# Performance work log

Measured on AMD Instinct MI355X. Metric: run time of the kernel, lower is better.

The kernel has to match this reference:

```python
import jax, jax.numpy as jnp
import numpy as np

NUM_EMBEDDINGS = 1024
EMBEDDING_DIM = 64
COMMITMENT_COST = 0.25


def setup_inputs() -> dict:
    key = jax.random.key(0)
    k1, k2 = jax.random.split(key)
    inputs = jax.random.normal(k1, (64, 32, 32, EMBEDDING_DIM), dtype=jnp.float32)
    # torch init is uniform(-1/K, 1/K); scale accordingly
    weight = jax.random.uniform(
        k2, (NUM_EMBEDDINGS, EMBEDDING_DIM), dtype=jnp.float32,
        minval=-1.0 / NUM_EMBEDDINGS, maxval=1.0 / NUM_EMBEDDINGS)
    return {"inputs": inputs, "weight": weight}


def reference(inputs, weight):
    input_shape = inputs.shape
    flat = inputs.reshape(-1, EMBEDDING_DIM)               # [N, D]
    distances = (jnp.sum(flat ** 2, axis=1, keepdims=True)
                 + jnp.sum(weight ** 2, axis=1)
                 - 2.0 * flat @ weight.T)                   # [N, K]
    encoding_indices = jnp.argmin(distances, axis=1)        # [N]
    # gather codes (equivalent to one-hot @ weight, but as a direct gather)
    quantized = weight[encoding_indices].reshape(input_shape)

    e_latent_loss = jnp.mean((jax.lax.stop_gradient(quantized) - inputs) ** 2)
    q_latent_loss = jnp.mean((quantized - jax.lax.stop_gradient(inputs)) ** 2)
    loss = q_latent_loss + COMMITMENT_COST * e_latent_loss

    # straight-through estimator
    quantized_ste = inputs + jax.lax.stop_gradient(quantized - inputs)

    # perplexity (equivalent to mean over the one-hot encodings)
    n_tokens = flat.shape[0]
    counts = jax.ops.segment_sum(
        jnp.ones((n_tokens,), jnp.float32), encoding_indices,
        num_segments=NUM_EMBEDDINGS)
    avg_probs = counts / n_tokens
    perplexity = jnp.exp(-jnp.sum(avg_probs * jnp.log(avg_probs + 1e-10)))

    indices_for_transformer = encoding_indices.reshape(input_shape[0], -1)
    return (loss, quantized_ste, perplexity, indices_for_transformer)
```

## Files before the change

### kernel.cpp

```cpp
#include <hip/hip_runtime.h>
#include <cstdint>
#include <cstddef>

#define N_TOKENS 65536
#define DIM 64
#define K_CODES 1024
#define NTH 256
#define TPB 128
#define NCH 16

#define OFF_Q 1
#define OFF_PERP 4194305
#define OFF_IDX 4194306

#define MARGIN 1.5e-4f

#define WS_LOSS   0
#define WS_FCNT   8
#define WS_COUNTS 16
#define WS_WHI    4112
#define WS_WLO    135184
#define WS_S2     266256
#define WS_FLIST  270352

typedef __attribute__((ext_vector_type(8))) short  s16x8;
typedef __attribute__((ext_vector_type(4))) float  f32x4;

__device__ __forceinline__ float fmulr(float a, float b){ return __fmul_rn(a,b); }
__device__ __forceinline__ float faddr(float a, float b){ return __fadd_rn(a,b); }

__device__ __forceinline__ unsigned short f2bf(float f) {
    unsigned u = __float_as_uint(f);
    unsigned r = u + 0x7fffu + ((u >> 16) & 1u);
    return (unsigned short)(r >> 16);
}
__device__ __forceinline__ float bf2f(unsigned short h) {
    return __uint_as_float(((unsigned)h) << 16);
}

__device__ float sumsq64_np(const float* __restrict__ p) {
    float s[16];
    #pragma unroll
    for (int l = 0; l < 16; ++l) {
        float a0 = fmulr(p[l],      p[l]);
        float a1 = fmulr(p[l + 16], p[l + 16]);
        float a2 = fmulr(p[l + 32], p[l + 32]);
        float a3 = fmulr(p[l + 48], p[l + 48]);
        s[l] = faddr(faddr(a0, a1), faddr(a2, a3));
    }
    #pragma unroll
    for (int len = 8; len >= 1; len >>= 1)
        #pragma unroll
        for (int l = 0; l < len; ++l)
            s[l] = faddr(s[l], s[l + len]);
    return s[0];
}

__device__ __forceinline__ void async_copy16(const void* g, void* l) {
    __builtin_amdgcn_global_load_lds(
        (const __attribute__((address_space(1))) void*)g,
        (__attribute__((address_space(3))) void*)l, 16, 0, 0);
}

__global__ void vq_prep(const float* __restrict__ W, unsigned short* __restrict__ Whi,
                        unsigned short* __restrict__ Wlo, float* __restrict__ s2g,
                        int* __restrict__ counts, int* __restrict__ gfcount,
                        double* __restrict__ loss_acc) {
    int gid = blockIdx.x * NTH + threadIdx.x;
    for (int e = gid; e < K_CODES * DIM; e += 16384) {
        float x = W[e];
        unsigned short hi = f2bf(x);
        unsigned short lo = f2bf(__fsub_rn(x, bf2f(hi)));
        int j = e >> 6, k = e & 63;
        int pos = j * 64 + (((k >> 3) ^ (j & 7)) << 3) + (k & 7);
        Whi[pos] = hi; Wlo[pos] = lo;
    }
    if (gid < K_CODES) { s2g[gid] = sumsq64_np(W + gid * 64); counts[gid] = 0; }
    if (gid == 0) { *loss_acc = 0.0; *gfcount = 0; }
}

__global__ __launch_bounds__(NTH, 2)
void vq_main(const float* __restrict__ X, const float* __restrict__ W,
             const unsigned short* __restrict__ WhiG, const unsigned short* __restrict__ WloG,
             const float* __restrict__ s2g, float* __restrict__ out,
             double* __restrict__ loss_acc, int* __restrict__ counts,
             int* __restrict__ gfcount, unsigned short* __restrict__ gflist) {
    __shared__ __align__(16) unsigned short xs_hi[TPB * 64];
    __shared__ __align__(16) unsigned short xs_lo[TPB * 64];
    __shared__ __align__(16) unsigned short ws_hi[2][64 * 64];
    __shared__ __align__(16) unsigned short ws_lo[2][64 * 64];
    __shared__ __align__(16) float s2s[K_CODES];
    __shared__ int fidx[TPB];
    __shared__ int flist[TPB];
    __shared__ int fcount, gbaseS;
    __shared__ double lred[4];

    const int tid  = threadIdx.x;
    const int lane = tid & 63, wave = tid >> 6;
    const int quad = lane >> 4, lrow = lane & 15;
    const int t0   = blockIdx.x * TPB;

    if (tid == 0) fcount = 0;

    {
        const char* gh = (const char*)WhiG;
        const char* gl = (const char*)WloG;
        char* lh = (char*)&ws_hi[0][0] + wave * 1024;
        char* ll = (char*)&ws_lo[0][0] + wave * 1024;
        #pragma unroll
        for (int i = 0; i < 2; ++i) {
            async_copy16(gh + i * 4096 + tid * 16, lh + i * 4096);
            async_copy16(gl + i * 4096 + tid * 16, ll + i * 4096);
        }
    }
    *(f32x4*)&s2s[tid * 4] = *(const f32x4*)&s2g[tid * 4];
    #pragma unroll
    for (int i = 0; i < 4; ++i) {
        int g = tid + NTH * i;
        int t = g >> 3, kb = g & 7;
        const float* src = X + (size_t)(t0 + t) * DIM + kb * 8;
        float v[8];
        *(f32x4*)v       = *(const f32x4*)src;
        *(f32x4*)(v + 4) = *(const f32x4*)(src + 4);
        unsigned short h[8], l[8];
        #pragma unroll
        for (int k = 0; k < 8; ++k) {
            h[k] = f2bf(v[k]);
            l[k] = f2bf(__fsub_rn(v[k], bf2f(h[k])));
        }
        int base = t * 64 + ((kb ^ (t & 7)) << 3);
        *(s16x8*)&xs_hi[base] = *(s16x8*)h;
        *(s16x8*)&xs_lo[base] = *(s16x8*)l;
    }
    __syncthreads();

    s16x8 a_h0[2], a_h1[2], a_l0[2], a_l1[2];
    #pragma unroll
    for (int rt = 0; rt < 2; ++rt) {
        int tf = wave * 32 + rt * 16 + lrow;
        int sA = tf & 7;
        a_h0[rt] = *(const s16x8*)&xs_hi[tf * 64 + (((0 + quad) ^ sA) << 3)];
        a_h1[rt] = *(const s16x8*)&xs_hi[tf * 64 + (((4 + quad) ^ sA) << 3)];
        a_l0[rt] = *(const s16x8*)&xs_lo[tf * 64 + (((0 + quad) ^ sA) << 3)];
        a_l1[rt] = *(const s16x8*)&xs_lo[tf * 64 + (((4 + quad) ^ sA) << 3)];
    }

    float r1v[8], r2v[8]; int r1i[8];
    #pragma unroll
    for (int ri = 0; ri < 8; ++ri) { r1v[ri] = 3.4e38f; r2v[ri] = 3.4e38f; r1i[ri] = 0x7fffffff; }

    for (int ch = 0; ch < NCH; ++ch) {
        const int buf = ch & 1;
        if (ch < NCH - 1) {
            const char* gh = (const char*)WhiG + (ch + 1) * 8192;
            const char* gl = (const char*)WloG + (ch + 1) * 8192;
            char* lh = (char*)&ws_hi[buf ^ 1][0] + wave * 1024;
            char* ll = (char*)&ws_lo[buf ^ 1][0] + wave * 1024;
            #pragma unroll
            for (int i = 0; i < 2; ++i) {
                async_copy16(gh + i * 4096 + tid * 16, lh + i * 4096);
                async_copy16(gl + i * 4096 + tid * 16, ll + i * 4096);
            }
        }
        #pragma unroll
        for (int ct = 0; ct < 4; ++ct) {
            int lc = ct * 16 + lrow;
            int sB = lrow & 7;
            const unsigned short* bh = &ws_hi[buf][lc * 64];
            const unsigned short* bl = &ws_lo[buf][lc * 64];
            s16x8 b_h0 = *(const s16x8*)&bh[((0 + quad) ^ sB) << 3];
            s16x8 b_h1 = *(const s16x8*)&bh[((4 + quad) ^ sB) << 3];
            s16x8 b_l0 = *(const s16x8*)&bl[((0 + quad) ^ sB) << 3];
            s16x8 b_l1 = *(const s16x8*)&bl[((4 + quad) ^ sB) << 3];
            int jcode = ch * 64 + lc;
            float s2v = s2s[jcode];
            float ainit = fmulr(-0.5f, s2v);
            #pragma unroll
            for (int rt = 0; rt < 2; ++rt) {
                f32x4 acc = {ainit, ainit, ainit, ainit};
                acc = __builtin_amdgcn_mfma_f32_16x16x32_bf16(a_h0[rt], b_h0, acc, 0, 0, 0);
                acc = __builtin_amdgcn_mfma_f32_16x16x32_bf16(a_h1[rt], b_h1, acc, 0, 0, 0);
                acc = __builtin_amdgcn_mfma_f32_16x16x32_bf16(a_h0[rt], b_l0, acc, 0, 0, 0);
                acc = __builtin_amdgcn_mfma_f32_16x16x32_bf16(a_h1[rt], b_l1, acc, 0, 0, 0);
                acc = __builtin_amdgcn_mfma_f32_16x16x32_bf16(a_l0[rt], b_h0, acc, 0, 0, 0);
                acc = __builtin_amdgcn_mfma_f32_16x16x32_bf16(a_l1[rt], b_h1, acc, 0, 0, 0);
                #pragma unroll
                for (int r = 0; r < 4; ++r) {
                    float d = fmulr(-2.0f, acc[r]);
                    int ri = rt * 4 + r;
                    bool lt = d < r1v[ri];
                    float sec = lt ? r1v[ri] : d;
                    r2v[ri] = fminf(r2v[ri], sec);
                    r1v[ri] = lt ? d : r1v[ri];
                    r1i[ri] = lt ? jcode : r1i[ri];
                }
            }
        }
        __syncthreads();
    }

    #pragma unroll
    for (int m = 1; m <= 8; m <<= 1) {
        #pragma unroll
        for (int ri = 0; ri < 8; ++ri) {
            float o1v = __shfl_xor(r1v[ri], m, 64);
            int   o1i = __shfl_xor(r1i[ri], m, 64);
            float o2v = __shfl_xor(r2v[ri], m, 64);
            bool take = (o1v < r1v[ri]) || (o1v == r1v[ri] && o1i < r1i[ri]);
            float loser = take ? r1v[ri] : o1v;
            r2v[ri] = fminf(fminf(r2v[ri], o2v), loser);
            if (take) { r1v[ri] = o1v; r1i[ri] = o1i; }
        }
    }
    if (lrow == 0) {
        #pragma unroll
        for (int ri = 0; ri < 8; ++ri) {
            int rt = ri >> 2, r = ri & 3;
            int t = wave * 32 + rt * 16 + quad * 4 + r;
            bool fb = (r2v[ri] - r1v[ri]) < MARGIN;
            fidx[t] = fb ? (r1i[ri] | (int)0x80000000) : r1i[ri];
            if (fb) { int p = atomicAdd(&fcount, 1); flist[p] = t; }
        }
    }
    __syncthreads();

    double lsum = 0.0;
    #pragma unroll
    for (int i = 0; i < 8; ++i) {
        int e4 = tid + NTH * i;
        int t = e4 >> 4, d4 = (e4 & 15) * 4;
        int iv = fidx[t];
        if (iv >= 0) {
            f32x4 q = *(const f32x4*)&W[iv * 64 + d4];
            f32x4 x = *(const f32x4*)&X[(size_t)(t0 + t) * 64 + d4];
            *(f32x4*)&out[(size_t)OFF_Q + (size_t)(t0 + t) * 64 + d4] = q;
            #pragma unroll
            for (int c = 0; c < 4; ++c) {
                float df = __fsub_rn(q[c], x[c]);
                lsum += (double)fmulr(df, df);
            }
        }
    }
    #pragma unroll
    for (int off = 32; off >= 1; off >>= 1) lsum += __shfl_down(lsum, off, 64);
    if (lane == 0) lred[wave] = lsum;
    if (tid < TPB) {
        int iv = fidx[tid];
        if (iv >= 0) {
            atomicAdd(&counts[iv], 1);
            out[(size_t)OFF_IDX + t0 + tid] = (float)iv;
        }
    }
    if (tid == 0) gbaseS = atomicAdd(gfcount, fcount);
    __syncthreads();
    if (tid < fcount) gflist[gbaseS + tid] = (unsigned short)(t0 + flist[tid]);
    if (tid == 0) atomicAdd(loss_acc, lred[0] + lred[1] + lred[2] + lred[3]);
}

__global__ __launch_bounds__(NTH, 3)
void vq_fallback(const float* __restrict__ X, const float* __restrict__ W,
                 const float* __restrict__ s2g, const int* __restrict__ gfcount,
                 const unsigned short* __restrict__ gflist, float* __restrict__ out,
                 double* __restrict__ loss_acc, int* __restrict__ counts) {
    int count = *gfcount;
    int base = blockIdx.x * 64;
    if (base >= count) return;
    int nt = min(64, count - base);

    __shared__ __align__(16) float xsf[64 * 64];
    __shared__ __align__(16) float wsf[128 * 64];
    __shared__ float s1f[64];
    __shared__ int gidx[64];
    __shared__ double lredf[4];

    const int tid = threadIdx.x;
    const int lane = tid & 63, wave = tid >> 6;
    const int r = tid & 15, c = tid >> 4;

    #pragma unroll
    for (int i = 0; i < 4; ++i) {
        int idx = tid + NTH * i;
        int t = idx >> 4, kb = idx & 15;
        int tok = gflist[base + (t < nt ? t : 0)];
        f32x4 v = *(const f32x4*)(X + (size_t)tok * 64 + kb * 4);
        *(f32x4*)&xsf[t * 64 + ((kb ^ ((t >> 2) & 7)) << 2)] = v;
    }
    if (tid < nt) s1f[tid] = sumsq64_np(X + (size_t)gflist[base + tid] * 64);

    float runVal[4]; int runIdx[4];
    #pragma unroll
    for (int i = 0; i < 4; ++i) { runVal[i] = 3.4e38f; runIdx[i] = 0; }

    for (int ch = 0; ch < 8; ++ch) {
        __syncthreads();
        #pragma unroll
        for (int i = 0; i < 8; ++i) {
            int idx = tid + NTH * i;
            int jl = idx >> 4, kb = idx & 15;
            f32x4 v = *(const f32x4*)(W + (size_t)(ch * 128 + jl) * 64 + kb * 4);
            *(f32x4*)&wsf[jl * 64 + ((kb ^ ((jl >> 3) & 7)) << 2)] = v;
        }
        __syncthreads();

        float acc[4][8];
        #pragma unroll
        for (int i = 0; i < 4; ++i)
            #pragma unroll
            for (int m = 0; m < 8; ++m) acc[i][m] = 0.0f;

        #pragma unroll
        for (int kb = 0; kb < 16; ++kb) {
            f32x4 xv[4], wv[8];
            #pragma unroll
            for (int i = 0; i < 4; ++i)
                xv[i] = *(const f32x4*)&xsf[(4 * r + i) * 64 + ((kb ^ (r & 7)) << 2)];
            #pragma unroll
            for (int m = 0; m < 8; ++m)
                wv[m] = *(const f32x4*)&wsf[(8 * c + m) * 64 + ((kb ^ (c & 7)) << 2)];
            #pragma unroll
            for (int i = 0; i < 4; ++i)
                #pragma unroll
                for (int m = 0; m < 8; ++m) {
                    acc[i][m] = __builtin_fmaf(xv[i][0], wv[m][0], acc[i][m]);
                    acc[i][m] = __builtin_fmaf(xv[i][1], wv[m][1], acc[i][m]);
                    acc[i][m] = __builtin_fmaf(xv[i][2], wv[m][2], acc[i][m]);
                    acc[i][m] = __builtin_fmaf(xv[i][3], wv[m][3], acc[i][m]);
                }
        }
        #pragma unroll
        for (int i = 0; i < 4; ++i) {
            float s1v = s1f[4 * r + i];
            #pragma unroll
            for (int m = 0; m < 8; ++m) {
                int jl = 8 * c + m;
                float d = faddr(faddr(s1v, s2g[ch * 128 + jl]), fmulr(-2.0f, acc[i][m]));
                if (d < runVal[i]) { runVal[i] = d; runIdx[i] = ch * 128 + jl; }
            }
        }
    }

    __syncthreads();
    unsigned long long* red = (unsigned long long*)wsf;
    #pragma unroll
    for (int i = 0; i < 4; ++i) {
        unsigned long long pk =
            ((unsigned long long)__float_as_uint(runVal[i]) << 32) |
            (unsigned long long)(unsigned int)runIdx[i];
        red[(4 * r + i) * 16 + c] = pk;
    }
    __syncthreads();
    if (tid < 64) {
        unsigned long long best = red[tid * 16];
        #pragma unroll
        for (int cc = 1; cc < 16; ++cc) {
            unsigned long long v = red[tid * 16 + cc];
            best = (v < best) ? v : best;
        }
        int idx = (int)(best & 0xffffffffu);
        gidx[tid] = idx;
        if (tid < nt) {
            int tok = gflist[base + tid];
            out[(size_t)OFF_IDX + tok] = (float)idx;
            atomicAdd(&counts[idx], 1);
        }
    }
    __syncthreads();
    double lsum = 0.0;
    #pragma unroll
    for (int i = 0; i < 4; ++i) {
        int e4 = tid + NTH * i;
        int t = e4 >> 4, d4 = (e4 & 15) * 4;
        if (t < nt) {
            int tok = gflist[base + t];
            int idx = gidx[t];
            f32x4 q = *(const f32x4*)&W[idx * 64 + d4];
            f32x4 x = *(const f32x4*)&X[(size_t)tok * 64 + d4];
            *(f32x4*)&out[(size_t)OFF_Q + (size_t)tok * 64 + d4] = q;
            #pragma unroll
            for (int cc = 0; cc < 4; ++cc) {
                float df = __fsub_rn(q[cc], x[cc]);
                lsum += (double)fmulr(df, df);
            }
        }
    }
    #pragma unroll
    for (int off = 32; off >= 1; off >>= 1) lsum += __shfl_down(lsum, off, 64);
    if (lane == 0) lredf[wave] = lsum;
    __syncthreads();
    if (tid == 0) atomicAdd(loss_acc, lredf[0] + lredf[1] + lredf[2] + lredf[3]);
}

__global__ void vq_final(const int* __restrict__ counts,
                         const double* __restrict__ loss_acc,
                         float* __restrict__ out) {
    __shared__ double hred[4];
    int tid = threadIdx.x;
    double h = 0.0;
    for (int j = tid; j < K_CODES; j += 256) {
        double p = (double)counts[j] / 65536.0;
        h += p * log(p + 1e-10);
    }
    #pragma unroll
    for (int off = 32; off >= 1; off >>= 1) h += __shfl_down(h, off, 64);
    if ((tid & 63) == 0) hred[tid >> 6] = h;
    __syncthreads();
    if (tid == 0) {
        double H = hred[0] + hred[1] + hred[2] + hred[3];
        out[OFF_PERP] = (float)exp(-H);
        double ls = *loss_acc;
        float Lf = (float)(ls / 4194304.0);
        out[0] = faddr(Lf, fmulr(0.25f, Lf));
    }
}

extern "C" void kernel_launch(void* const* d_in, const int* in_sizes, int n_in,
                              void* d_out, int out_size, void* d_ws, size_t ws_size,
                              hipStream_t stream) {
    const float* X = (const float*)d_in[0];
    const float* W = (const float*)d_in[1];
    float* out = (float*)d_out;
    char* ws = (char*)d_ws;
    double* loss_acc = (double*)(ws + WS_LOSS);
    int* gfcount = (int*)(ws + WS_FCNT);
    int* counts = (int*)(ws + WS_COUNTS);
    unsigned short* Whi = (unsigned short*)(ws + WS_WHI);
    unsigned short* Wlo = (unsigned short*)(ws + WS_WLO);
    float* s2g = (float*)(ws + WS_S2);
    unsigned short* gflist = (unsigned short*)(ws + WS_FLIST);

    vq_prep<<<64, NTH, 0, stream>>>(W, Whi, Wlo, s2g, counts, gfcount, loss_acc);
    vq_main<<<N_TOKENS / TPB, NTH, 0, stream>>>(X, W, Whi, Wlo, s2g, out,
                                                loss_acc, counts, gfcount, gflist);
    vq_fallback<<<N_TOKENS / 64, NTH, 0, stream>>>(X, W, s2g, gfcount, gflist,
                                                   out, loss_acc, counts);
    vq_final<<<1, NTH, 0, stream>>>(counts, loss_acc, out);
}
```

Baseline: 173.2 us.

## Split codebook across two wave groups per block and track max dot

The main kernel grows from 256 to 512 threads. Each group of four waves scans half of every 64-code chunk for the same 128 tokens, and the two halves are merged in shared memory. The per-code multiply by -2 is dropped by tracking the maximum of the offset dot product, with the margin halved to match. This doubles the waves available to hide MFMA and LDS latency at the cost of an extra shared-memory merge, a barrier, and more register pressure under the stricter launch bound.

```diff
diff --git a/kernel.cpp b/kernel.cpp
--- a/kernel.cpp
+++ b/kernel.cpp
@@ -6,6 +6,7 @@
 #define DIM 64
 #define K_CODES 1024
 #define NTH 256
+#define NTHM 512
 #define TPB 128
 #define NCH 16
 
@@ -14,6 +15,7 @@
 #define OFF_IDX 4194306
 
 #define MARGIN 1.5e-4f
+#define HMARGIN 7.5e-5f
 
 #define WS_LOSS   0
 #define WS_FCNT   8
@@ -79,7 +81,7 @@
     if (gid == 0) { *loss_acc = 0.0; *gfcount = 0; }
 }
 
-__global__ __launch_bounds__(NTH, 2)
+__global__ __launch_bounds__(NTHM, 4)
 void vq_main(const float* __restrict__ X, const float* __restrict__ W,
              const unsigned short* __restrict__ WhiG, const unsigned short* __restrict__ WloG,
              const float* __restrict__ s2g, float* __restrict__ out,
@@ -90,14 +92,19 @@
     __shared__ __align__(16) unsigned short ws_hi[2][64 * 64];
     __shared__ __align__(16) unsigned short ws_lo[2][64 * 64];
     __shared__ __align__(16) float s2s[K_CODES];
+    __shared__ float sm1[2][TPB];
+    __shared__ float sm2[2][TPB];
+    __shared__ int   si1[2][TPB];
     __shared__ int fidx[TPB];
     __shared__ int flist[TPB];
     __shared__ int fcount, gbaseS;
-    __shared__ double lred[4];
+    __shared__ double lred[8];
 
     const int tid  = threadIdx.x;
     const int lane = tid & 63, wave = tid >> 6;
     const int quad = lane >> 4, lrow = lane & 15;
+    const int tg   = wave & 3;
+    const int chd  = wave >> 2;
     const int t0   = blockIdx.x * TPB;
 
     if (tid == 0) fcount = 0;
@@ -107,16 +114,13 @@
         const char* gl = (const char*)WloG;
         char* lh = (char*)&ws_hi[0][0] + wave * 1024;
         char* ll = (char*)&ws_lo[0][0] + wave * 1024;
-        #pragma unroll
-        for (int i = 0; i < 2; ++i) {
-            async_copy16(gh + i * 4096 + tid * 16, lh + i * 4096);
-            async_copy16(gl + i * 4096 + tid * 16, ll + i * 4096);
-        }
-    }
-    *(f32x4*)&s2s[tid * 4] = *(const f32x4*)&s2g[tid * 4];
-    #pragma unroll
-    for (int i = 0; i < 4; ++i) {
-        int g = tid + NTH * i;
+        async_copy16(gh + tid * 16, lh);
+        async_copy16(gl + tid * 16, ll);
+    }
+    if (tid < 256) *(f32x4*)&s2s[tid * 4] = *(const f32x4*)&s2g[tid * 4];
+    #pragma unroll
+    for (int i = 0; i < 2; ++i) {
+        int g = tid + NTHM * i;
         int t = g >> 3, kb = g & 7;
         const float* src = X + (size_t)(t0 + t) * DIM + kb * 8;
         float v[8];
@@ -137,7 +141,7 @@
     s16x8 a_h0[2], a_h1[2], a_l0[2], a_l1[2];
     #pragma unroll
     for (int rt = 0; rt < 2; ++rt) {
-        int tf = wave * 32 + rt * 16 + lrow;
+        int tf = tg * 32 + rt * 16 + lrow;
         int sA = tf & 7;
         a_h0[rt] = *(const s16x8*)&xs_hi[tf * 64 + (((0 + quad) ^ sA) << 3)];
         a_h1[rt] = *(const s16x8*)&xs_hi[tf * 64 + (((4 + quad) ^ sA) << 3)];
@@ -145,9 +149,9 @@
         a_l1[rt] = *(const s16x8*)&xs_lo[tf * 64 + (((4 + quad) ^ sA) << 3)];
     }
 
-    float r1v[8], r2v[8]; int r1i[8];
-    #pragma unroll
-    for (int ri = 0; ri < 8; ++ri) { r1v[ri] = 3.4e38f; r2v[ri] = 3.4e38f; r1i[ri] = 0x7fffffff; }
+    float m1v[8], m2v[8]; int m1i[8];
+    #pragma unroll
+    for (int ri = 0; ri < 8; ++ri) { m1v[ri] = -3.4e38f; m2v[ri] = -3.4e38f; m1i[ri] = 0x7fffffff; }
 
     for (int ch = 0; ch < NCH; ++ch) {
         const int buf = ch & 1;
@@ -156,15 +160,12 @@
             const char* gl = (const char*)WloG + (ch + 1) * 8192;
             char* lh = (char*)&ws_hi[buf ^ 1][0] + wave * 1024;
             char* ll = (char*)&ws_lo[buf ^ 1][0] + wave * 1024;
-            #pragma unroll
-            for (int i = 0; i < 2; ++i) {
-                async_copy16(gh + i * 4096 + tid * 16, lh + i * 4096);
-                async_copy16(gl + i * 4096 + tid * 16, ll + i * 4096);
-            }
-        }
-        #pragma unroll
-        for (int ct = 0; ct < 4; ++ct) {
-            int lc = ct * 16 + lrow;
+            async_copy16(gh + tid * 16, lh);
+            async_copy16(gl + tid * 16, ll);
+        }
+        #pragma unroll
+        for (int ct2 = 0; ct2 < 2; ++ct2) {
+            int lc = chd * 32 + ct2 * 16 + lrow;
             int sB = lrow & 7;
             const unsigned short* bh = &ws_hi[buf][lc * 64];
             const unsigned short* bl = &ws_lo[buf][lc * 64];
@@ -186,13 +187,13 @@
                 acc = __builtin_amdgcn_mfma_f32_16x16x32_bf16(a_l1[rt], b_h1, acc, 0, 0, 0);
                 #pragma unroll
                 for (int r = 0; r < 4; ++r) {
-                    float d = fmulr(-2.0f, acc[r]);
+                    float a = acc[r];
                     int ri = rt * 4 + r;
-                    bool lt = d < r1v[ri];
-                    float sec = lt ? r1v[ri] : d;
-                    r2v[ri] = fminf(r2v[ri], sec);
-                    r1v[ri] = lt ? d : r1v[ri];
-                    r1i[ri] = lt ? jcode : r1i[ri];
+                    bool gt = a > m1v[ri];
+                    float sec = gt ? m1v[ri] : a;
+                    m2v[ri] = fmaxf(m2v[ri], sec);
+                    m1v[ri] = gt ? a : m1v[ri];
+                    m1i[ri] = gt ? jcode : m1i[ri];
                 }
             }
         }
@@ -203,31 +204,46 @@
     for (int m = 1; m <= 8; m <<= 1) {
         #pragma unroll
         for (int ri = 0; ri < 8; ++ri) {
-            float o1v = __shfl_xor(r1v[ri], m, 64);
-            int   o1i = __shfl_xor(r1i[ri], m, 64);
-            float o2v = __shfl_xor(r2v[ri], m, 64);
-            bool take = (o1v < r1v[ri]) || (o1v == r1v[ri] && o1i < r1i[ri]);
-            float loser = take ? r1v[ri] : o1v;
-            r2v[ri] = fminf(fminf(r2v[ri], o2v), loser);
-            if (take) { r1v[ri] = o1v; r1i[ri] = o1i; }
+            float o1v = __shfl_xor(m1v[ri], m, 64);
+            int   o1i = __shfl_xor(m1i[ri], m, 64);
+            float o2v = __shfl_xor(m2v[ri], m, 64);
+            bool take = (o1v > m1v[ri]) || (o1v == m1v[ri] && o1i < m1i[ri]);
+            float loser = take ? m1v[ri] : o1v;
+            m2v[ri] = fmaxf(fmaxf(m2v[ri], o2v), loser);
+            if (take) { m1v[ri] = o1v; m1i[ri] = o1i; }
         }
     }
     if (lrow == 0) {
         #pragma unroll
         for (int ri = 0; ri < 8; ++ri) {
             int rt = ri >> 2, r = ri & 3;
-            int t = wave * 32 + rt * 16 + quad * 4 + r;
-            bool fb = (r2v[ri] - r1v[ri]) < MARGIN;
-            fidx[t] = fb ? (r1i[ri] | (int)0x80000000) : r1i[ri];
-            if (fb) { int p = atomicAdd(&fcount, 1); flist[p] = t; }
-        }
+            int t = tg * 32 + rt * 16 + quad * 4 + r;
+            sm1[chd][t] = m1v[ri];
+            sm2[chd][t] = m2v[ri];
+            si1[chd][t] = m1i[ri];
+        }
+    }
+    __syncthreads();
+    if (tid < TPB) {
+        int t = tid;
+        float a1 = sm1[0][t], b1 = sm1[1][t];
+        int   ia = si1[0][t], ib = si1[1][t];
+        float a2 = sm2[0][t], b2 = sm2[1][t];
+        bool take = (b1 > a1) || (b1 == a1 && ib < ia);
+        float w1 = take ? b1 : a1;
+        int   wi = take ? ib : ia;
+        float loser = take ? a1 : b1;
+        float w2 = fmaxf(fmaxf(a2, b2), loser);
+        bool fb = __fsub_rn(w1, w2) < HMARGIN;
+        fidx[t] = fb ? (wi | (int)0x80000000) : wi;
+        if (fb) { int p = atomicAdd(&fcount, 1); flist[p] = t; }
     }
     __syncthreads();
 
     double lsum = 0.0;
     #pragma unroll
-    for (int i = 0; i < 8; ++i) {
-        int e4 = tid + NTH * i;
+    for (int i = 0; i < 4; ++i) {
+        int e4 = tid + NTHM * i;
         int t = e4 >> 4, d4 = (e4 & 15) * 4;
         int iv = fidx[t];
         if (iv >= 0) {
@@ -254,7 +270,9 @@
     if (tid == 0) gbaseS = atomicAdd(gfcount, fcount);
     __syncthreads();
     if (tid < fcount) gflist[gbaseS + tid] = (unsigned short)(t0 + flist[tid]);
-    if (tid == 0) atomicAdd(loss_acc, lred[0] + lred[1] + lred[2] + lred[3]);
+    if (tid == 0)
+        atomicAdd(loss_acc, lred[0] + lred[1] + lred[2] + lred[3] +
+                            lred[4] + lred[5] + lred[6] + lred[7]);
 }
 
 __global__ __launch_bounds__(NTH, 3)
@@ -429,8 +447,8 @@
     unsigned short* gflist = (unsigned short*)(ws + WS_FLIST);
 
     vq_prep<<<64, NTH, 0, stream>>>(W, Whi, Wlo, s2g, counts, gfcount, loss_acc);
-    vq_main<<<N_TOKENS / TPB, NTH, 0, stream>>>(X, W, Whi, Wlo, s2g, out,
-                                                loss_acc, counts, gfcount, gflist);
+    vq_main<<<N_TOKENS / TPB, NTHM, 0, stream>>>(X, W, Whi, Wlo, s2g, out,
+                                                 loss_acc, counts, gfcount, gflist);
     vq_fallback<<<N_TOKENS / 64, NTH, 0, stream>>>(X, W, s2g, gfcount, gflist,
                                                    out, loss_acc, counts);
     vq_final<<<1, NTH, 0, stream>>>(counts, loss_acc, out);
```

After: 166.0 us. 4.2% less time.
